# Optimization experiments

Measured on AMD Instinct MI355X. Metric: run time of the kernel, lower is better.

## Reference

```python
import jax, jax.numpy as jnp
import numpy as np

N_HEAD = 16
N_KV_HEAD = 4
D_HEAD = 128
RMS_EPS = 1.1920929e-07  # torch default eps for fp32 rms_norm


def _rms_norm(x):
    return x * jax.lax.rsqrt(jnp.mean(x * x, axis=-1, keepdims=True) + RMS_EPS)


def _rotary_tables(n_pos, dim):
    # dim = d_head; freq table has dim//2 entries (half of them zero)
    angular_freq = (1.0 / 1024.0) ** jnp.linspace(0.0, 1.0, dim // 4, dtype=jnp.float32)
    angular_freq = jnp.concatenate([angular_freq, jnp.zeros(dim // 4, jnp.float32)])
    theta = jnp.arange(n_pos, dtype=jnp.float32)[:, None] * angular_freq[None, :]
    return jnp.cos(theta), jnp.sin(theta)


def _apply_rotary(x):
    # x: (B, H, T, D). Faithful to source: cos/sin indexed by x.shape[-3] (= H),
    # broadcast over the time axis.
    n = x.shape[-3]
    cos, sin = _rotary_tables(n, x.shape[-1])
    cos = cos[None, :, None, :]
    sin = sin[None, :, None, :]
    xf = x.astype(jnp.float32)
    x1, x2 = jnp.split(xf, 2, axis=-1)
    y1 = x1 * cos + x2 * sin
    y2 = -x1 * sin + x2 * cos
    return jnp.concatenate([y1, y2], axis=-1).astype(x.dtype)


def setup_inputs() -> dict:
    key = jax.random.key(0)
    k1, k2, k3, k4 = jax.random.split(key, 4)
    B, T, C = 2, 2048, 2048
    return {
        "x": jax.random.normal(k1, (B, T, C), jnp.float32),
        "Wq": jax.random.normal(k2, (C, C), jnp.float32) * 0.02,
        "Wkv": jax.random.normal(k3, (2 * N_KV_HEAD * D_HEAD, C), jnp.float32) * 0.02,
        "Wproj": jax.random.normal(k4, (C, C), jnp.float32) * 0.02,
        "tok_masks": jnp.ones((B, T), jnp.int32),
    }


def reference(x, Wq, Wkv, Wproj, tok_masks):
    B, T, C = x.shape
    nh, nkv, dh = N_HEAD, N_KV_HEAD, D_HEAD

    q = (x @ Wq.T).reshape(B, T, nh, dh).transpose(0, 2, 1, 3)          # (B,nh,T,dh)
    kv = x @ Wkv.T                                                       # (B,T,2*nkv*dh)
    k, v = jnp.split(kv, 2, axis=2)
    k = k.reshape(B, T, nkv, dh).transpose(0, 2, 1, 3)                   # (B,nkv,T,dh)
    v = v.reshape(B, T, nkv, dh).transpose(0, 2, 1, 3)

    q, k = _rms_norm(q), _rms_norm(k)
    q, k = _apply_rotary(q), _apply_rotary(k)

    # GQA: repeat kv heads to match query heads
    rep = nh // nkv
    k = jnp.repeat(k, rep, axis=1)
    v = jnp.repeat(v, rep, axis=1)

    scale = 1.0 / jnp.sqrt(jnp.float32(dh))
    scores = jnp.einsum("bhqd,bhkd->bhqk", q, k) * scale                 # (B,nh,T,T)
    causal = jnp.tril(jnp.ones((T, T), bool))
    scores = jnp.where(causal[None, None], scores, -jnp.inf)
    attn = jax.nn.softmax(scores, axis=-1)
    y = jnp.einsum("bhqk,bhkd->bhqd", attn, v)                           # (B,nh,T,dh)
    y = y.transpose(0, 2, 1, 3).reshape(B, T, C)
    y = y @ Wproj.T
    return (y, jnp.float32(0.0))
```

## Files before the change

### kernel.cpp

```cpp
#include <hip/hip_runtime.h>
#include <hip/hip_bf16.h>

#define T_SEQ 2048
#define BATCH 2
#define CDIM  2048
#define NH    16
#define NKV   4
#define DH    128

typedef __attribute__((ext_vector_type(8))) short bfrag;
typedef __attribute__((ext_vector_type(4))) short bhalf;
typedef __attribute__((ext_vector_type(4))) float ffrag;
typedef __hip_bfloat16 bf16;

__device__ __forceinline__ void gll16(const bf16* __restrict__ g, bf16* lds) {
    __builtin_amdgcn_global_load_lds((const __attribute__((address_space(1))) void*)g,
                                     (__attribute__((address_space(3))) void*)lds, 16, 0, 0);
}

__device__ __forceinline__ unsigned cvt_pk_bf16(float lo, float hi) {
    unsigned r;
    asm("v_cvt_pk_bf16_f32 %0, %1, %2" : "=v"(r) : "v"(lo), "v"(hi));
    return r;
}

struct bf16x4 { bf16 a, b, c, d; };
#define N4_X   (BATCH * T_SEQ * CDIM / 4)
#define N4_WQ  (CDIM * CDIM / 4)
#define N4_WKV (2 * NKV * DH * CDIM / 4)
#define N4_WP  (CDIM * CDIM / 4)
__global__ __launch_bounds__(256) void cast_all(
    const float* __restrict__ x, const float* __restrict__ wq,
    const float* __restrict__ wkv, const float* __restrict__ wp,
    bf16* __restrict__ xb, bf16* __restrict__ wqb, bf16* __restrict__ wkvb, bf16* __restrict__ wpb)
{
    int j = blockIdx.x * 256 + threadIdx.x;
    const float* s; bf16* d;
    if (j < N4_X) { s = x; d = xb; }
    else {
        j -= N4_X;
        if (j < N4_WQ) { s = wq; d = wqb; }
        else {
            j -= N4_WQ;
            if (j < N4_WKV) { s = wkv; d = wkvb; }
            else { j -= N4_WKV; if (j >= N4_WP) return; s = wp; d = wpb; }
        }
    }
    float4 f = ((const float4*)s)[j];
    bf16x4 o{__float2bfloat16(f.x), __float2bfloat16(f.y),
             __float2bfloat16(f.z), __float2bfloat16(f.w)};
    ((bf16x4*)d)[j] = o;
}

template<int MODE>
__device__ __forceinline__ void gemm_body(
    const bf16* __restrict__ A, const bf16* __restrict__ W, int m0, int n0,
    bf16* __restrict__ out0, bf16* __restrict__ out1, float* __restrict__ outf)
{
    __shared__ __align__(16) bf16 sA[64 * 64];
    __shared__ __align__(16) bf16 sB[64 * 64];

    const int lane = threadIdx.x & 63;
    const int w    = threadIdx.x >> 6;
    const int wm   = w >> 1, wn = w & 1;
    const int lr   = lane & 15, quad = lane >> 4;

    const int pr8  = lane >> 3;
    const int ls   = (lane & 7) ^ pr8;
    const int rloc = 2 * (w * 8 + pr8) + (ls >> 2);
    const int k0s  = (ls & 3) * 8;

    const bf16* Aj0 = A + (size_t)(m0 +      rloc) * CDIM + k0s;
    const bf16* Aj1 = A + (size_t)(m0 + 64 + rloc) * CDIM + k0s;
    const bf16* Bj0 = W + (size_t)(n0 +      rloc) * CDIM + k0s;
    const bf16* Bj1 = W + (size_t)(n0 + 64 + rloc) * CDIM + k0s;
    bf16* dA0 = sA +        w * 512;
    bf16* dA1 = sA + 2048 + w * 512;
    bf16* dB0 = sB +        w * 512;
    bf16* dB1 = sB + 2048 + w * 512;

    const int soff = ((((lr & 1) << 2) | quad) ^ ((lr >> 1) & 7)) << 3;

    ffrag acc[4][4] = {};
    for (int kk = 0; kk < CDIM; kk += 32) {
        __syncthreads();
        gll16(Aj0 + kk, dA0);
        gll16(Aj1 + kk, dA1);
        gll16(Bj0 + kk, dB0);
        gll16(Bj1 + kk, dB1);
        __syncthreads();

        bfrag af[4], bg[4];
        #pragma unroll
        for (int f = 0; f < 4; ++f)
            af[f] = *(const bfrag*)&sA[((f * 16 + wm * 8 + (lr >> 1)) << 6) + soff];
        #pragma unroll
        for (int g = 0; g < 4; ++g)
            bg[g] = *(const bfrag*)&sB[((g * 16 + wn * 8 + (lr >> 1)) << 6) + soff];
        #pragma unroll
        for (int f = 0; f < 4; ++f)
            #pragma unroll
            for (int g = 0; g < 4; ++g)
                acc[f][g] = __builtin_amdgcn_mfma_f32_16x16x32_bf16(af[f], bg[g], acc[f][g], 0, 0, 0);
    }

    #pragma unroll
    for (int f = 0; f < 4; ++f) {
        #pragma unroll
        for (int g = 0; g < 4; ++g) {
            #pragma unroll
            for (int i = 0; i < 4; ++i) {
                const int m = m0 + f * 32 + wm * 16 + quad * 4 + i;
                const int n = n0 + g * 32 + wn * 16 + lr;
                const float v = acc[f][g][i];
                if constexpr (MODE == 0) {
                    int b = m >> 11, t = m & (T_SEQ - 1);
                    int h = n >> 7, d = n & (DH - 1);
                    out0[(((size_t)(b * NH + h) * T_SEQ + t) << 7) + d] = __float2bfloat16(v);
                } else if constexpr (MODE == 1) {
                    int b = m >> 11, t = m & (T_SEQ - 1);
                    if (n < NKV * DH) {
                        int h = n >> 7, d = n & (DH - 1);
                        out0[(((size_t)(b * NKV + h) * T_SEQ + t) << 7) + d] = __float2bfloat16(v);
                    } else {
                        int n2 = n - NKV * DH;
                        int h = n2 >> 7, d = n2 & (DH - 1);
                        out1[(((size_t)(b * NKV + h) * DH + d) << 11) + t] = __float2bfloat16(v);
                    }
                } else {
                    outf[(size_t)m * CDIM + n] = v;
                }
            }
        }
    }
}

__global__ __launch_bounds__(256) void gemm_qkv(
    const bf16* __restrict__ A, const bf16* __restrict__ Wq, const bf16* __restrict__ Wkv,
    bf16* __restrict__ q, bf16* __restrict__ k, bf16* __restrict__ vt)
{
    if (blockIdx.y < 16)
        gemm_body<0>(A, Wq, blockIdx.x * 128, blockIdx.y * 128, q, nullptr, nullptr);
    else
        gemm_body<1>(A, Wkv, blockIdx.x * 128, (blockIdx.y - 16) * 128, k, vt, nullptr);
}

__global__ __launch_bounds__(256) void gemm_proj(
    const bf16* __restrict__ A, const bf16* __restrict__ W, float* __restrict__ outf)
{
    gemm_body<2>(A, W, blockIdx.x * 128, blockIdx.y * 128, nullptr, nullptr, outf);
    if (blockIdx.x == 0 && blockIdx.y == 0 && threadIdx.x == 0)
        outf[(size_t)BATCH * T_SEQ * CDIM] = 0.0f;
}

#define QROWS (BATCH * NH * T_SEQ)
#define KROWS (BATCH * NKV * T_SEQ)
__global__ __launch_bounds__(256) void normrope_k(bf16* __restrict__ qb, bf16* __restrict__ kb) {
    int row = blockIdx.x * 4 + (threadIdx.x >> 6);
    bf16* bufb; int nheads;
    if (row < QROWS) { bufb = qb; nheads = NH; }
    else { row -= QROWS; bufb = kb; nheads = NKV; }
    const int h = (row >> 11) % nheads;
    bf16* p = bufb + (size_t)row * DH;
    const int d = threadIdx.x & 63;
    float x1 = __bfloat162float(p[d]);
    float x2 = __bfloat162float(p[d + 64]);
    float ss = x1 * x1 + x2 * x2;
    #pragma unroll
    for (int off = 32; off; off >>= 1) ss += __shfl_xor(ss, off);
    float r = rsqrtf(ss * (1.0f / 128.0f) + 1.1920929e-07f);
    x1 *= r; x2 *= r;
    float freq = (d < 32) ? exp2f(-10.0f * (float)d * (1.0f / 31.0f)) : 0.0f;
    float th = (float)h * freq;
    float c, s;
    __sincosf(th, &s, &c);
    p[d]      = __float2bfloat16(x1 * c + x2 * s);
    p[d + 64] = __float2bfloat16(-x1 * s + x2 * c);
}

__global__ __launch_bounds__(512, 2) void attn_k(const bf16* __restrict__ Q, const bf16* __restrict__ K,
                                                 const bf16* __restrict__ VT, bf16* __restrict__ Y)
{
    const int lane = threadIdx.x & 63;
    const int w = threadIdx.x >> 6;
    const int g = w >> 2, wl = w & 3;
    const int p = blockIdx.x, h = blockIdx.y, b = blockIdx.z;
    const int lr = lane & 15, quad = lane >> 4, lk = quad * 8;
    const bf16* Qb = Q  + (size_t)(b * NH  + h)        * T_SEQ * DH;
    const bf16* Kb = K  + (size_t)(b * NKV + (h >> 2)) * T_SEQ * DH;
    const bf16* Vb = VT + (size_t)(b * NKV + (h >> 2)) * DH * T_SEQ;

    __shared__ __align__(16) union ShmU {
        struct { bf16 SK[2][2][32 * 128]; bf16 SV[2][2][128 * 32]; } s;
        ffrag MRG[9 * 4 * 64];
    } shm;

    const int k_r0 = wl * 8 + (lane >> 4);
    const int k_ch = lane & 15;
    const int v_r0 = wl * 32 + (lane >> 2);
    const int v_ch = lane & 3;
    const int vsw = (lr + (lr >> 2)) & 3;
    const float scale = 0.08838834764831845f;

    auto load_v_perm = [&](const bf16* rp) {
        union { bhalf h[2]; bfrag f; } u;
        u.h[0] = *(const bhalf*)(rp + v_ch * 4);
        u.h[1] = *(const bhalf*)(rp + 16 + v_ch * 4);
        return u.f;
    };

    for (int pass = 0; pass < 2; ++pass) {
        const int qb = pass ? (15 - p) : p;
        const int nc = 2 * (qb + 1);
        const int q0 = qb * 128 + wl * 32;

        bfrag qf[2][4];
        #pragma unroll
        for (int t = 0; t < 2; ++t)
            #pragma unroll
            for (int dc = 0; dc < 4; ++dc)
                qf[t][dc] = *(const bfrag*)(Qb + (size_t)(q0 + t * 16 + lr) * DH + dc * 32 + lk);

        float lp[2] = {};
        ffrag o[2][8] = {};

        bfrag kr[2], vr[2];
        {
            const int b0 = g * 32;
            #pragma unroll
            for (int j = 0; j < 2; ++j) {
                kr[j] = *(const bfrag*)(Kb + (size_t)(b0 + k_r0 + j * 4) * DH + k_ch * 8);
                vr[j] = load_v_perm(Vb + (size_t)(v_r0 + j * 16) * T_SEQ + b0);
            }
            #pragma unroll
            for (int j = 0; j < 2; ++j) {
                int krow = k_r0 + j * 4;
                *(bfrag*)&shm.s.SK[g][0][krow * 128 + ((k_ch ^ (krow & 15))) * 8] = kr[j];
                int vrow = v_r0 + j * 16;
                *(bfrag*)&shm.s.SV[g][0][vrow * 32 + ((v_ch ^ ((vrow + (vrow >> 2)) & 3))) * 8] = vr[j];
            }
            if (nc > 1) {
                const int nb = 64 + g * 32;
                #pragma unroll
                for (int j = 0; j < 2; ++j) {
                    kr[j] = *(const bfrag*)(Kb + (size_t)(nb + k_r0 + j * 4) * DH + k_ch * 8);
                    vr[j] = load_v_perm(Vb + (size_t)(v_r0 + j * 16) * T_SEQ + nb);
                }
            }
        }
        __syncthreads();

        for (int c = 0; c < nc; ++c) {
            const int cur = c & 1, nxt = cur ^ 1;
            const int base = c * 64 + g * 32;
            const bf16* SKc = shm.s.SK[g][cur];
            const bf16* SVc = shm.s.SV[g][cur];

            if (c + 1 < nc) {
                #pragma unroll
                for (int j = 0; j < 2; ++j) {
                    int krow = k_r0 + j * 4;
                    *(bfrag*)&shm.s.SK[g][nxt][krow * 128 + ((k_ch ^ (krow & 15))) * 8] = kr[j];
                    int vrow = v_r0 + j * 16;
                    *(bfrag*)&shm.s.SV[g][nxt][vrow * 32 + ((v_ch ^ ((vrow + (vrow >> 2)) & 3))) * 8] = vr[j];
                }
                if (c + 2 < nc) {
                    const int nb = (c + 2) * 64 + g * 32;
                    #pragma unroll
                    for (int j = 0; j < 2; ++j) {
                        kr[j] = *(const bfrag*)(Kb + (size_t)(nb + k_r0 + j * 4) * DH + k_ch * 8);
                        vr[j] = load_v_perm(Vb + (size_t)(v_r0 + j * 16) * T_SEQ + nb);
                    }
                }
            }

            ffrag s2[2][2] = {};
            #pragma unroll
            for (int kt = 0; kt < 2; ++kt)
                #pragma unroll
                for (int dc = 0; dc < 4; ++dc) {
                    bfrag kf = *(const bfrag*)&SKc[(kt * 16 + lr) * 128 + (((dc << 2) | quad) ^ lr) * 8];
                    s2[0][kt] = __builtin_amdgcn_mfma_f32_16x16x32_bf16(kf, qf[0][dc], s2[0][kt], 0, 0, 0);
                    s2[1][kt] = __builtin_amdgcn_mfma_f32_16x16x32_bf16(kf, qf[1][dc], s2[1][kt], 0, 0, 0);
                }

            const bool maskc = (c >= 2 * qb);
            bfrag pf[2];
            #pragma unroll
            for (int t = 0; t < 2; ++t) {
                const int qa = q0 + t * 16 + lr;
                float ev[2][4];
                #pragma unroll
                for (int kt = 0; kt < 2; ++kt)
                    #pragma unroll
                    for (int i = 0; i < 4; ++i) {
                        const int ka = base + kt * 16 + quad * 4 + i;
                        float e = (!maskc || ka <= qa) ? __expf(fmaf(s2[t][kt][i], scale, -16.0f)) : 0.0f;
                        lp[t] += e;
                        ev[kt][i] = e;
                    }
                union { unsigned u[4]; bfrag f; } pu;
                pu.u[0] = cvt_pk_bf16(ev[0][0], ev[0][1]);
                pu.u[1] = cvt_pk_bf16(ev[0][2], ev[0][3]);
                pu.u[2] = cvt_pk_bf16(ev[1][0], ev[1][1]);
                pu.u[3] = cvt_pk_bf16(ev[1][2], ev[1][3]);
                pf[t] = pu.f;
            }

            #pragma unroll
            for (int dt = 0; dt < 8; ++dt) {
                bfrag vf = *(const bfrag*)&SVc[(dt * 16 + lr) * 32 + ((quad ^ vsw)) * 8];
                o[0][dt] = __builtin_amdgcn_mfma_f32_16x16x32_bf16(pf[0], vf, o[0][dt], 0, 0, 0);
                o[1][dt] = __builtin_amdgcn_mfma_f32_16x16x32_bf16(pf[1], vf, o[1][dt], 0, 0, 0);
            }

            __syncthreads();
        }

        __syncthreads();
        #pragma unroll
        for (int t = 0; t < 2; ++t) {
            if (g == 1) {
                #pragma unroll
                for (int d = 0; d < 8; ++d) shm.MRG[(d * 4 + wl) * 64 + lane] = o[t][d];
                ffrag l4 = {lp[t], 0.0f, 0.0f, 0.0f};
                shm.MRG[(8 * 4 + wl) * 64 + lane] = l4;
            }
            __syncthreads();
            if (g == 0) {
                #pragma unroll
                for (int d = 0; d < 8; ++d) o[t][d] += shm.MRG[(d * 4 + wl) * 64 + lane];
                float lsum = lp[t] + shm.MRG[(8 * 4 + wl) * 64 + lane][0];
                lsum += __shfl_xor(lsum, 16);
                lsum += __shfl_xor(lsum, 32);
                float inv[4];
                #pragma unroll
                for (int i = 0; i < 4; ++i)
                    inv[i] = 1.0f / __shfl(lsum, quad * 4 + i);
                #pragma unroll
                for (int dt = 0; dt < 8; ++dt)
                    #pragma unroll
                    for (int i = 0; i < 4; ++i) {
                        int row = q0 + t * 16 + quad * 4 + i;
                        Y[((size_t)(b * T_SEQ) + row) * CDIM + h * DH + dt * 16 + lr] =
                            __float2bfloat16(o[t][dt][i] * inv[i]);
                    }
            }
            __syncthreads();
        }
    }
}

extern "C" void kernel_launch(void* const* d_in, const int* in_sizes, int n_in,
                              void* d_out, int out_size, void* d_ws, size_t ws_size,
                              hipStream_t stream) {
    const float* x     = (const float*)d_in[0];
    const float* Wq    = (const float*)d_in[1];
    const float* Wkv   = (const float*)d_in[2];
    const float* Wproj = (const float*)d_in[3];
    float* out = (float*)d_out;

    char* ws = (char*)d_ws;
    size_t off = 0;
    auto alloc = [&](size_t bytes) { void* p = ws + off; off += (bytes + 255) & ~255ULL; return p; };
    bf16* xb   = (bf16*)alloc((size_t)BATCH * T_SEQ * CDIM * 2);
    bf16* wqb  = (bf16*)alloc((size_t)CDIM * CDIM * 2);
    bf16* wkvb = (bf16*)alloc((size_t)2 * NKV * DH * CDIM * 2);
    bf16* wpb  = (bf16*)alloc((size_t)CDIM * CDIM * 2);
    bf16* qb   = (bf16*)alloc((size_t)BATCH * NH * T_SEQ * DH * 2);
    bf16* kb   = (bf16*)alloc((size_t)BATCH * NKV * T_SEQ * DH * 2);
    bf16* vtb  = (bf16*)alloc((size_t)BATCH * NKV * DH * T_SEQ * 2);
    bf16* y1   = (bf16*)alloc((size_t)BATCH * T_SEQ * CDIM * 2);

    const int total4 = N4_X + N4_WQ + N4_WKV + N4_WP;
    cast_all<<<(total4 + 255) / 256, 256, 0, stream>>>(x, Wq, Wkv, Wproj, xb, wqb, wkvb, wpb);

    gemm_qkv<<<dim3(32, 24), 256, 0, stream>>>(xb, wqb, wkvb, qb, kb, vtb);
    normrope_k<<<(QROWS + KROWS) / 4, 256, 0, stream>>>(qb, kb);
    attn_k<<<dim3(8, NH, BATCH), 512, 0, stream>>>(qb, kb, vtb, y1);
    gemm_proj<<<dim3(32, 16), 256, 0, stream>>>(y1, wpb, out);
}
```

Before: 301.0 us.

## Fuse RMS norm and rotary embedding into QKV GEMM epilogue

Removes the separate normrope kernel and applies per-head RMS normalization and rotary rotation directly on the GEMM accumulators before storing Q and K. Each 128-wide N tile is one head, so the row sum of squares is reduced with lane shuffles plus a small shared-memory exchange between the two column-wave halves. The K and V column tiles are split into separate template modes so that only Q/K tiles get the normalization. This saves a full read and write pass over Q and K and one kernel launch, at the cost of an extra barrier and epilogue work in the GEMM. It also normalizes the fp32 accumulators before the bf16 rounding rather than after.

```diff
diff --git a/kernel.cpp b/kernel.cpp
--- a/kernel.cpp
+++ b/kernel.cpp
@@ -55,11 +55,9 @@
 template<int MODE>
 __device__ __forceinline__ void gemm_body(
     const bf16* __restrict__ A, const bf16* __restrict__ W, int m0, int n0,
-    bf16* __restrict__ out0, bf16* __restrict__ out1, float* __restrict__ outf)
+    bf16* __restrict__ out0, bf16* __restrict__ out1, float* __restrict__ outf,
+    bf16* __restrict__ sA, bf16* __restrict__ sB, float (* __restrict__ hb)[128])
 {
-    __shared__ __align__(16) bf16 sA[64 * 64];
-    __shared__ __align__(16) bf16 sB[64 * 64];
-
     const int lane = threadIdx.x & 63;
     const int w    = threadIdx.x >> 6;
     const int wm   = w >> 1, wn = w & 1;
@@ -102,6 +100,45 @@
             #pragma unroll
             for (int g = 0; g < 4; ++g)
                 acc[f][g] = __builtin_amdgcn_mfma_f32_16x16x32_bf16(af[f], bg[g], acc[f][g], 0, 0, 0);
+    }
+
+    if constexpr (MODE == 0 || MODE == 1) {
+        float ssh[4][4];
+        #pragma unroll
+        for (int f = 0; f < 4; ++f)
+            #pragma unroll
+            for (int i = 0; i < 4; ++i) {
+                float ss = acc[f][0][i] * acc[f][0][i] + acc[f][1][i] * acc[f][1][i]
+                         + acc[f][2][i] * acc[f][2][i] + acc[f][3][i] * acc[f][3][i];
+                #pragma unroll
+                for (int off = 1; off < 16; off <<= 1) ss += __shfl_xor(ss, off);
+                ssh[f][i] = ss;
+            }
+        if (lr == 0) {
+            #pragma unroll
+            for (int f = 0; f < 4; ++f)
+                #pragma unroll
+                for (int i = 0; i < 4; ++i)
+                    hb[wn][f * 32 + wm * 16 + quad * 4 + i] = ssh[f][i];
+        }
+        __syncthreads();
+        const int h_angle = n0 >> 7;
+        const float freq = exp2f(-10.0f * (float)(wn * 16 + lr) * (1.0f / 31.0f));
+        float sn, cs;
+        __sincosf((float)h_angle * freq, &sn, &cs);
+        #pragma unroll
+        for (int f = 0; f < 4; ++f)
+            #pragma unroll
+            for (int i = 0; i < 4; ++i) {
+                float ss = ssh[f][i] + hb[wn ^ 1][f * 32 + wm * 16 + quad * 4 + i];
+                float r = rsqrtf(ss * (1.0f / 128.0f) + 1.1920929e-07f);
+                float x0 = acc[f][0][i] * r, x1 = acc[f][1][i] * r;
+                float x2 = acc[f][2][i] * r, x3 = acc[f][3][i] * r;
+                acc[f][0][i] =  x0 * cs + x2 * sn;
+                acc[f][2][i] = -x0 * sn + x2 * cs;
+                acc[f][1][i] = x1;
+                acc[f][3][i] = x3;
+            }
     }
 
     #pragma unroll
@@ -119,14 +156,13 @@
                     out0[(((size_t)(b * NH + h) * T_SEQ + t) << 7) + d] = __float2bfloat16(v);
                 } else if constexpr (MODE == 1) {
                     int b = m >> 11, t = m & (T_SEQ - 1);
-                    if (n < NKV * DH) {
-                        int h = n >> 7, d = n & (DH - 1);
-                        out0[(((size_t)(b * NKV + h) * T_SEQ + t) << 7) + d] = __float2bfloat16(v);
-                    } else {
-                        int n2 = n - NKV * DH;
-                        int h = n2 >> 7, d = n2 & (DH - 1);
-                        out1[(((size_t)(b * NKV + h) * DH + d) << 11) + t] = __float2bfloat16(v);
-                    }
+                    int h = n >> 7, d = n & (DH - 1);
+                    out0[(((size_t)(b * NKV + h) * T_SEQ + t) << 7) + d] = __float2bfloat16(v);
+                } else if constexpr (MODE == 3) {
+                    int b = m >> 11, t = m & (T_SEQ - 1);
+                    int n2 = n - NKV * DH;
+                    int h = n2 >> 7, d = n2 & (DH - 1);
+                    out1[(((size_t)(b * NKV + h) * DH + d) << 11) + t] = __float2bfloat16(v);
                 } else {
                     outf[(size_t)m * CDIM + n] = v;
                 }
@@ -139,43 +175,27 @@
     const bf16* __restrict__ A, const bf16* __restrict__ Wq, const bf16* __restrict__ Wkv,
     bf16* __restrict__ q, bf16* __restrict__ k, bf16* __restrict__ vt)
 {
-    if (blockIdx.y < 16)
-        gemm_body<0>(A, Wq, blockIdx.x * 128, blockIdx.y * 128, q, nullptr, nullptr);
+    __shared__ __align__(16) bf16 sA[64 * 64];
+    __shared__ __align__(16) bf16 sB[64 * 64];
+    __shared__ float hb[2][128];
+    const int y = blockIdx.y;
+    if (y < 16)
+        gemm_body<0>(A, Wq,  blockIdx.x * 128, y * 128,        q, nullptr, nullptr, sA, sB, hb);
+    else if (y < 20)
+        gemm_body<1>(A, Wkv, blockIdx.x * 128, (y - 16) * 128, k, nullptr, nullptr, sA, sB, hb);
     else
-        gemm_body<1>(A, Wkv, blockIdx.x * 128, (blockIdx.y - 16) * 128, k, vt, nullptr);
+        gemm_body<3>(A, Wkv, blockIdx.x * 128, (y - 16) * 128, nullptr, vt, nullptr, sA, sB, hb);
 }
 
 __global__ __launch_bounds__(256) void gemm_proj(
     const bf16* __restrict__ A, const bf16* __restrict__ W, float* __restrict__ outf)
 {
-    gemm_body<2>(A, W, blockIdx.x * 128, blockIdx.y * 128, nullptr, nullptr, outf);
+    __shared__ __align__(16) bf16 sA[64 * 64];
+    __shared__ __align__(16) bf16 sB[64 * 64];
+    gemm_body<2>(A, W, blockIdx.x * 128, blockIdx.y * 128, nullptr, nullptr, outf,
+                 sA, sB, nullptr);
     if (blockIdx.x == 0 && blockIdx.y == 0 && threadIdx.x == 0)
         outf[(size_t)BATCH * T_SEQ * CDIM] = 0.0f;
-}
-
-#define QROWS (BATCH * NH * T_SEQ)
-#define KROWS (BATCH * NKV * T_SEQ)
-__global__ __launch_bounds__(256) void normrope_k(bf16* __restrict__ qb, bf16* __restrict__ kb) {
-    int row = blockIdx.x * 4 + (threadIdx.x >> 6);
-    bf16* bufb; int nheads;
-    if (row < QROWS) { bufb = qb; nheads = NH; }
-    else { row -= QROWS; bufb = kb; nheads = NKV; }
-    const int h = (row >> 11) % nheads;
-    bf16* p = bufb + (size_t)row * DH;
-    const int d = threadIdx.x & 63;
-    float x1 = __bfloat162float(p[d]);
-    float x2 = __bfloat162float(p[d + 64]);
-    float ss = x1 * x1 + x2 * x2;
-    #pragma unroll
-    for (int off = 32; off; off >>= 1) ss += __shfl_xor(ss, off);
-    float r = rsqrtf(ss * (1.0f / 128.0f) + 1.1920929e-07f);
-    x1 *= r; x2 *= r;
-    float freq = (d < 32) ? exp2f(-10.0f * (float)d * (1.0f / 31.0f)) : 0.0f;
-    float th = (float)h * freq;
-    float c, s;
-    __sincosf(th, &s, &c);
-    p[d]      = __float2bfloat16(x1 * c + x2 * s);
-    p[d + 64] = __float2bfloat16(-x1 * s + x2 * c);
 }
 
 __global__ __launch_bounds__(512, 2) void attn_k(const bf16* __restrict__ Q, const bf16* __restrict__ K,
@@ -376,7 +396,6 @@
     cast_all<<<(total4 + 255) / 256, 256, 0, stream>>>(x, Wq, Wkv, Wproj, xb, wqb, wkvb, wpb);
 
     gemm_qkv<<<dim3(32, 24), 256, 0, stream>>>(xb, wqb, wkvb, qb, kb, vtb);
-    normrope_k<<<(QROWS + KROWS) / 4, 256, 0, stream>>>(qb, kb);
     attn_k<<<dim3(8, NH, BATCH), 512, 0, stream>>>(qb, kb, vtb, y1);
     gemm_proj<<<dim3(32, 16), 256, 0, stream>>>(y1, wpb, out);
 }
```

After: 307.9 us. 2.3% more time.
